# Performance work log

Hardware: AMD Instinct MI355X
Metric: run time of the kernel (lower is better)

The kernel has to match this reference:

```python
import jax, jax.numpy as jnp
import numpy as np

N = 50000      # nodes
E = 800000     # edges (avg degree 16)
D_IN = 128
D_H = 256
NUM_LAYERS = 5


def setup_inputs() -> dict:
    key = jax.random.key(0)
    ks = jax.random.split(key, 12)
    s_in = 1.0 / np.sqrt(D_IN)
    s_h = 1.0 / np.sqrt(D_H)
    x = jax.random.normal(ks[0], (N, D_IN), jnp.float32)
    edge_index = jax.random.randint(ks[1], (2, E), 0, N, jnp.int32)
    eps_all = jnp.zeros((NUM_LAYERS,), jnp.float32)
    # torch Linear layout: weight [out, in], y = x @ W.T + b; scaled for stability
    w0_l0 = jax.random.normal(ks[2], (D_H, D_IN), jnp.float32) * s_in
    b0_l0 = jax.random.normal(ks[3], (D_H,), jnp.float32) * 0.01
    w1_l0 = jax.random.normal(ks[4], (D_H, D_H), jnp.float32) * s_h
    b1_l0 = jax.random.normal(ks[5], (D_H,), jnp.float32) * 0.01
    w0_rest = jax.random.normal(ks[6], (4, D_H, D_H), jnp.float32) * s_h
    b0_rest = jax.random.normal(ks[7], (4, D_H), jnp.float32) * 0.01
    w1_rest = jax.random.normal(ks[8], (4, D_H, D_H), jnp.float32) * s_h
    b1_rest = jax.random.normal(ks[9], (4, D_H), jnp.float32) * 0.01
    return {"x": x, "edge_index": edge_index, "eps_all": eps_all,
            "w0_l0": w0_l0, "b0_l0": b0_l0, "w1_l0": w1_l0, "b1_l0": b1_l0,
            "w0_rest": w0_rest, "b0_rest": b0_rest, "w1_rest": w1_rest, "b1_rest": b1_rest}


def _gin_layer(x, src, dst, eps, w0, b0, w1, b1):
    # gather source-node features along edges, scatter-sum into destination nodes
    aggr = jax.ops.segment_sum(x[src], dst, num_segments=N)  # [N, d]
    h = (1.0 + eps) * x + aggr
    h = jax.nn.relu(h @ w0.T + b0)   # dropout p=0.0 -> identity
    h = h @ w1.T + b1
    return jax.nn.relu(h)            # inter-layer ReLU from the trace


def reference(x, edge_index, eps_all, w0_l0, b0_l0, w1_l0, b1_l0,
              w0_rest, b0_rest, w1_rest, b1_rest):
    src = edge_index[0]  # edge_index_j (messages come from row 0)
    dst = edge_index[1]  # edge_index_i (aggregated at row 1)
    h = _gin_layer(x, src, dst, eps_all[0], w0_l0, b0_l0, w1_l0, b1_l0)
    for i in range(4):  # layers 1..4, identical shapes
        h = _gin_layer(h, src, dst, eps_all[i + 1],
                       w0_rest[i], b0_rest[i], w1_rest[i], b1_rest[i])
    return h  # [N, D_H]
```

## Files before the change

### kernel.cpp

```cpp
#include <hip/hip_runtime.h>
#include <hip/hip_bf16.h>
#include <stdint.h>

#define D_IN 128
#define D_H 256
#define NLAYERS 5

typedef __bf16 bf16x8 __attribute__((ext_vector_type(8)));
typedef float f32x4 __attribute__((ext_vector_type(4)));
typedef unsigned short u16x8 __attribute__((ext_vector_type(8)));

#define MID_STRIDE 260

__device__ inline unsigned short bfbits(float f) {
  __hip_bfloat16 h = __float2bfloat16(f);
  unsigned short s;
  __builtin_memcpy(&s, &h, 2);
  return s;
}

__device__ inline unsigned packbf(float lo, float hi) {
  return (unsigned)bfbits(lo) | ((unsigned)bfbits(hi) << 16);
}

__device__ inline void addbf2(float& a, float& b, unsigned u) {
  a += __uint_as_float(u << 16);
  b += __uint_as_float(u & 0xffff0000u);
}

__device__ inline void addbf2s(float& a, float& b, unsigned u, float s) {
  a += s * __uint_as_float(u << 16);
  b += s * __uint_as_float(u & 0xffff0000u);
}

__global__ void conv_inputs(const float* __restrict__ x, const float* __restrict__ a,
                            const float* __restrict__ b, const float* __restrict__ c,
                            const float* __restrict__ d,
                            __hip_bfloat16* __restrict__ xb,
                            __hip_bfloat16* __restrict__ wb, int nx) {
  int gid = blockIdx.x * blockDim.x + threadIdx.x;
  if (gid < nx) {
    xb[gid] = __float2bfloat16(x[gid]);
    return;
  }
  gid -= nx;
  if (gid >= 622592) return;
  float v;
  if (gid < 32768) v = a[gid];
  else if (gid < 98304) v = b[gid - 32768];
  else if (gid < 360448) v = c[gid - 98304];
  else v = d[gid - 360448];
  wb[gid] = __float2bfloat16(v);
}

__global__ void zero_ints(int* __restrict__ p, int n) {
  int i = blockIdx.x * blockDim.x + threadIdx.x;
  if (i < n) p[i] = 0;
}

__global__ void hist_kernel(const int* __restrict__ ei, int E, int* __restrict__ deg) {
  int e = blockIdx.x * blockDim.x + threadIdx.x;
  if (e < E) atomicAdd(&deg[ei[E + e]], 1);
}

__global__ __launch_bounds__(256) void block_sums(const int* __restrict__ deg,
                                                  int* __restrict__ bsum, int N) {
  int t = threadIdx.x;
  int idx = blockIdx.x * 1024 + t * 4;
  int4 v = {0, 0, 0, 0};
  if (idx + 3 < N) v = *reinterpret_cast<const int4*>(deg + idx);
  else {
    if (idx + 0 < N) v.x = deg[idx + 0];
    if (idx + 1 < N) v.y = deg[idx + 1];
    if (idx + 2 < N) v.z = deg[idx + 2];
    if (idx + 3 < N) v.w = deg[idx + 3];
  }
  int s = v.x + v.y + v.z + v.w;
#pragma unroll
  for (int off = 32; off > 0; off >>= 1) s += __shfl_down(s, off);
  __shared__ int ws[4];
  int lane = t & 63, w = t >> 6;
  if (lane == 0) ws[w] = s;
  __syncthreads();
  if (t == 0) bsum[blockIdx.x] = ws[0] + ws[1] + ws[2] + ws[3];
}

__global__ void scan_bsums(int* __restrict__ bsum, int nb) {
  int t = threadIdx.x;
  int orig = (t < nb) ? bsum[t] : 0;
  int v = orig;
#pragma unroll
  for (int off = 1; off < 64; off <<= 1) {
    int u = __shfl_up(v, off);
    if (t >= off) v += u;
  }
  if (t < nb) bsum[t] = v - orig;
}

__global__ __launch_bounds__(256) void scan_apply(const int* __restrict__ deg,
                                                  const int* __restrict__ bsum_ex,
                                                  int* __restrict__ row_start, int N) {
  int t = threadIdx.x;
  int idx = blockIdx.x * 1024 + t * 4;
  int4 v = {0, 0, 0, 0};
  if (idx + 3 < N) v = *reinterpret_cast<const int4*>(deg + idx);
  else {
    if (idx + 0 < N) v.x = deg[idx + 0];
    if (idx + 1 < N) v.y = deg[idx + 1];
    if (idx + 2 < N) v.z = deg[idx + 2];
    if (idx + 3 < N) v.w = deg[idx + 3];
  }
  int s = v.x + v.y + v.z + v.w;
  int lane = t & 63, w = t >> 6;
  int sc = s;
#pragma unroll
  for (int off = 1; off < 64; off <<= 1) {
    int u = __shfl_up(sc, off);
    if (lane >= off) sc += u;
  }
  __shared__ int woff[4];
  if (lane == 63) woff[w] = sc;
  __syncthreads();
  int boff = bsum_ex[blockIdx.x];
#pragma unroll
  for (int i = 0; i < 4; ++i)
    if (i < w) boff += woff[i];
  int ex = boff + sc - s;
  if (idx + 3 < N) {
    int4 o;
    o.x = ex;
    o.y = ex + v.x;
    o.z = ex + v.x + v.y;
    o.w = ex + v.x + v.y + v.z;
    *reinterpret_cast<int4*>(row_start + idx) = o;
  } else {
    if (idx + 0 < N) row_start[idx + 0] = ex;
    if (idx + 1 < N) row_start[idx + 1] = ex + v.x;
    if (idx + 2 < N) row_start[idx + 2] = ex + v.x + v.y;
    if (idx + 3 < N) row_start[idx + 3] = ex + v.x + v.y + v.z;
  }
}

__global__ void fill_kernel(const int* __restrict__ ei, int E,
                            const int* __restrict__ row_start,
                            int* __restrict__ cursor, int* __restrict__ csr) {
  int e = blockIdx.x * blockDim.x + threadIdx.x;
  if (e >= E) return;
  int d = ei[E + e];
  int p = atomicAdd(&cursor[d], 1);
  csr[row_start[d] + p] = ei[e];
}

template <int D>
__global__ __launch_bounds__(256) void aggregate(const unsigned short* __restrict__ hb,
                                                 const int* __restrict__ csr,
                                                 const int* __restrict__ row_start,
                                                 const int* __restrict__ deg,
                                                 const float* __restrict__ eps_all,
                                                 int layer,
                                                 unsigned short* __restrict__ pre,
                                                 int N) {
  constexpr int PL = D / 32;
  const int half = threadIdx.x >> 5;
  const int lane = threadIdx.x & 31;
  const int node = blockIdx.x * 8 + half;
  if (node >= N) return;

  const int start = row_start[node];
  const int cnt = deg[node];
  const float epsv = 1.0f + eps_all[layer];

  float acc[PL];
#pragma unroll
  for (int j = 0; j < PL; ++j) acc[j] = 0.0f;

  if (D == 256) {
    uint4 su = *reinterpret_cast<const uint4*>(hb + (size_t)node * D + lane * 8);
    for (int base = 0; base < cnt; base += 32) {
      int m = cnt - base;
      if (m > 32) m = 32;
      int idx = (lane < m) ? csr[start + base + lane] : 0;
      int i = 0;
      for (; i + 8 <= m; i += 8) {
        uint4 q[8];
#pragma unroll
        for (int r = 0; r < 8; ++r) {
          int s = __shfl(idx, i + r, 32);
          q[r] = *reinterpret_cast<const uint4*>(hb + (size_t)s * D + lane * 8);
        }
#pragma unroll
        for (int r = 0; r < 8; ++r) {
          addbf2(acc[0], acc[1], q[r].x);
          addbf2(acc[2], acc[3], q[r].y);
          addbf2(acc[4], acc[5], q[r].z);
          addbf2(acc[6], acc[7], q[r].w);
        }
      }
      for (; i + 4 <= m; i += 4) {
        uint4 q[4];
#pragma unroll
        for (int r = 0; r < 4; ++r) {
          int s = __shfl(idx, i + r, 32);
          q[r] = *reinterpret_cast<const uint4*>(hb + (size_t)s * D + lane * 8);
        }
#pragma unroll
        for (int r = 0; r < 4; ++r) {
          addbf2(acc[0], acc[1], q[r].x);
          addbf2(acc[2], acc[3], q[r].y);
          addbf2(acc[4], acc[5], q[r].z);
          addbf2(acc[6], acc[7], q[r].w);
        }
      }
      for (; i < m; ++i) {
        int s = __shfl(idx, i, 32);
        uint4 q = *reinterpret_cast<const uint4*>(hb + (size_t)s * D + lane * 8);
        addbf2(acc[0], acc[1], q.x);
        addbf2(acc[2], acc[3], q.y);
        addbf2(acc[4], acc[5], q.z);
        addbf2(acc[6], acc[7], q.w);
      }
    }
    addbf2s(acc[0], acc[1], su.x, epsv);
    addbf2s(acc[2], acc[3], su.y, epsv);
    addbf2s(acc[4], acc[5], su.z, epsv);
    addbf2s(acc[6], acc[7], su.w, epsv);
    uint4 o;
    o.x = packbf(acc[0], acc[1]);
    o.y = packbf(acc[2], acc[3]);
    o.z = packbf(acc[4], acc[5]);
    o.w = packbf(acc[6], acc[7]);
    *reinterpret_cast<uint4*>(pre + (size_t)node * D + lane * 8) = o;
  } else {
    uint2 su = *reinterpret_cast<const uint2*>(hb + (size_t)node * D + lane * 4);
    for (int base = 0; base < cnt; base += 32) {
      int m = cnt - base;
      if (m > 32) m = 32;
      int idx = (lane < m) ? csr[start + base + lane] : 0;
      int i = 0;
      for (; i + 8 <= m; i += 8) {
        uint2 q[8];
#pragma unroll
        for (int r = 0; r < 8; ++r) {
          int s = __shfl(idx, i + r, 32);
          q[r] = *reinterpret_cast<const uint2*>(hb + (size_t)s * D + lane * 4);
        }
#pragma unroll
        for (int r = 0; r < 8; ++r) {
          addbf2(acc[0], acc[1], q[r].x);
          addbf2(acc[2], acc[3], q[r].y);
        }
      }
      for (; i + 4 <= m; i += 4) {
        uint2 q[4];
#pragma unroll
        for (int r = 0; r < 4; ++r) {
          int s = __shfl(idx, i + r, 32);
          q[r] = *reinterpret_cast<const uint2*>(hb + (size_t)s * D + lane * 4);
        }
#pragma unroll
        for (int r = 0; r < 4; ++r) {
          addbf2(acc[0], acc[1], q[r].x);
          addbf2(acc[2], acc[3], q[r].y);
        }
      }
      for (; i < m; ++i) {
        int s = __shfl(idx, i, 32);
        uint2 q = *reinterpret_cast<const uint2*>(hb + (size_t)s * D + lane * 4);
        addbf2(acc[0], acc[1], q.x);
        addbf2(acc[2], acc[3], q.y);
      }
    }
    addbf2s(acc[0], acc[1], su.x, epsv);
    addbf2s(acc[2], acc[3], su.y, epsv);
    uint2 o;
    o.x = packbf(acc[0], acc[1]);
    o.y = packbf(acc[2], acc[3]);
    *reinterpret_cast<uint2*>(pre + (size_t)node * D + lane * 4) = o;
  }
}

template <int K0, bool OUT_BF16>
__global__ __launch_bounds__(512, 2) void mlp_fused(
    const unsigned short* __restrict__ Ap, const __hip_bfloat16* __restrict__ W0p,
    const float* __restrict__ b0, const __hip_bfloat16* __restrict__ W1p,
    const float* __restrict__ b1, void* __restrict__ Outp, int Nrows) {
  __shared__ unsigned short midb[2][32 * MID_STRIDE];

  constexpr int NK0 = K0 / 32;
  constexpr int NK1 = D_H / 32;
  const int tid = threadIdx.x;
  const int wid = tid >> 6;
  const bool prod = (wid < 4);
  const int cg = wid & 3;
  const int lane = tid & 63;
  const int l15 = lane & 15;
  const int kg = lane >> 4;
  const int col0 = cg * 64;
  const int nch = (Nrows + 31) >> 5;

  bf16x8 wfr[NK1][4];
  float bv[4];
  if (prod) {
    const unsigned short* Ws = (const unsigned short*)W0p;
#pragma unroll
    for (int ct = 0; ct < 4; ++ct) {
      const unsigned short* wrow = Ws + (size_t)(col0 + ct * 16 + l15) * K0 + kg * 8;
#pragma unroll
      for (int kk = 0; kk < NK0; ++kk)
        wfr[kk][ct] = *reinterpret_cast<const bf16x8*>(wrow + kk * 32);
      bv[ct] = b0[col0 + ct * 16 + l15];
    }
  } else {
    const unsigned short* Ws = (const unsigned short*)W1p;
#pragma unroll
    for (int ct = 0; ct < 4; ++ct) {
      const unsigned short* wrow = Ws + (size_t)(col0 + ct * 16 + l15) * D_H + kg * 8;
#pragma unroll
      for (int kk = 0; kk < NK1; ++kk)
        wfr[kk][ct] = *reinterpret_cast<const bf16x8*>(wrow + kk * 32);
      bv[ct] = b1[col0 + ct * 16 + l15];
    }
  }

  auto produce = [&](int c, unsigned short* buf) {
    const int r0 = c << 5;
    bf16x8 afr[NK0][2];
#pragma unroll
    for (int rt = 0; rt < 2; ++rt) {
      int row = r0 + rt * 16 + l15;
      if (row > Nrows - 1) row = Nrows - 1;
      const unsigned short* ar = Ap + (size_t)row * K0 + kg * 8;
#pragma unroll
      for (int kk = 0; kk < NK0; ++kk)
        afr[kk][rt] = *reinterpret_cast<const bf16x8*>(ar + kk * 32);
    }
    f32x4 acc[2][4];
#pragma unroll
    for (int rt = 0; rt < 2; ++rt)
#pragma unroll
      for (int ct = 0; ct < 4; ++ct) acc[rt][ct] = 0.0f;
#pragma unroll
    for (int kk = 0; kk < NK0; ++kk)
#pragma unroll
      for (int rt = 0; rt < 2; ++rt)
#pragma unroll
        for (int ct = 0; ct < 4; ++ct)
          acc[rt][ct] = __builtin_amdgcn_mfma_f32_16x16x32_bf16(
              afr[kk][rt], wfr[kk][ct], acc[rt][ct], 0, 0, 0);
#pragma unroll
    for (int ct = 0; ct < 4; ++ct) {
      int col = col0 + ct * 16 + l15;
#pragma unroll
      for (int rt = 0; rt < 2; ++rt)
#pragma unroll
        for (int i = 0; i < 4; ++i) {
          int row_l = rt * 16 + kg * 4 + i;
          buf[row_l * MID_STRIDE + col] = bfbits(fmaxf(acc[rt][ct][i] + bv[ct], 0.0f));
        }
    }
  };

  auto consume = [&](int c, const unsigned short* buf) {
    const int r0 = c << 5;
    f32x4 acc[2][4];
#pragma unroll
    for (int rt = 0; rt < 2; ++rt)
#pragma unroll
      for (int ct = 0; ct < 4; ++ct) acc[rt][ct] = 0.0f;
#pragma unroll
    for (int kk = 0; kk < NK1; ++kk) {
      bf16x8 mfr[2];
#pragma unroll
      for (int rt = 0; rt < 2; ++rt)
        mfr[rt] = *reinterpret_cast<const bf16x8*>(
            buf + (rt * 16 + l15) * MID_STRIDE + kk * 32 + kg * 8);
#pragma unroll
      for (int rt = 0; rt < 2; ++rt)
#pragma unroll
        for (int ct = 0; ct < 4; ++ct)
          acc[rt][ct] = __builtin_amdgcn_mfma_f32_16x16x32_bf16(
              mfr[rt], wfr[kk][ct], acc[rt][ct], 0, 0, 0);
    }
#pragma unroll
    for (int ct = 0; ct < 4; ++ct) {
      int col = col0 + ct * 16 + l15;
#pragma unroll
      for (int rt = 0; rt < 2; ++rt)
#pragma unroll
        for (int i = 0; i < 4; ++i) {
          int row = r0 + rt * 16 + kg * 4 + i;
          if (row < Nrows) {
            float v = fmaxf(acc[rt][ct][i] + bv[ct], 0.0f);
            if (OUT_BF16)
              ((__hip_bfloat16*)Outp)[(size_t)row * D_H + col] = __float2bfloat16(v);
            else
              ((float*)Outp)[(size_t)row * D_H + col] = v;
          }
        }
    }
  };

  int c_pr = blockIdx.x;
  int c_co = blockIdx.x;
  int pb = 0;
  if (prod && c_pr < nch) produce(c_pr, midb[0]);
  __syncthreads();
  c_pr += gridDim.x;
  while (c_co < nch) {
    if (prod) {
      if (c_pr < nch) produce(c_pr, midb[pb ^ 1]);
    } else {
      consume(c_co, midb[pb]);
    }
    __syncthreads();
    pb ^= 1;
    c_pr += gridDim.x;
    c_co += gridDim.x;
  }
}

extern "C" void kernel_launch(void* const* d_in, const int* in_sizes, int n_in,
                              void* d_out, int out_size, void* d_ws, size_t ws_size,
                              hipStream_t stream) {
  const float* x = (const float*)d_in[0];
  const int* ei = (const int*)d_in[1];
  const float* eps_all = (const float*)d_in[2];
  const float* w0_l0 = (const float*)d_in[3];
  const float* b0_l0 = (const float*)d_in[4];
  const float* w1_l0 = (const float*)d_in[5];
  const float* b1_l0 = (const float*)d_in[6];
  const float* w0_rest = (const float*)d_in[7];
  const float* b0_rest = (const float*)d_in[8];
  const float* w1_rest = (const float*)d_in[9];
  const float* b1_rest = (const float*)d_in[10];

  const int N = in_sizes[0] / D_IN;
  const int E = in_sizes[1] / 2;
  const int NX = N * D_IN;

  char* ws = (char*)d_ws;
  const size_t node_bf = (size_t)N * D_H * sizeof(unsigned short);
  unsigned short* h = (unsigned short*)ws;
  unsigned short* pre = (unsigned short*)(ws + node_bf);
  unsigned short* xb = (unsigned short*)(ws + 2 * node_bf);
  char* p = ws + 2 * node_bf + (size_t)NX * sizeof(unsigned short);
  __hip_bfloat16* wbf = (__hip_bfloat16*)p;
  p += 622592 * sizeof(__hip_bfloat16);
  int* deg = (int*)p;
  int* cursor = deg + N;
  int* row_start = cursor + N;
  int* bsum = row_start + N;
  int* csr = bsum + 64;

  __hip_bfloat16* w0_l0_bf = wbf;
  __hip_bfloat16* w1_l0_bf = wbf + 32768;
  __hip_bfloat16* w0_rest_bf = wbf + 98304;
  __hip_bfloat16* w1_rest_bf = w0_rest_bf + 262144;

  conv_inputs<<<(NX + 622592 + 255) / 256, 256, 0, stream>>>(
      x, w0_l0, w1_l0, w0_rest, w1_rest, (__hip_bfloat16*)xb, wbf, NX);

  const int nb = (N + 1023) / 1024;
  zero_ints<<<(2 * N + 255) / 256, 256, 0, stream>>>(deg, 2 * N);
  hist_kernel<<<(E + 255) / 256, 256, 0, stream>>>(ei, E, deg);
  block_sums<<<nb, 256, 0, stream>>>(deg, bsum, N);
  scan_bsums<<<1, 64, 0, stream>>>(bsum, nb);
  scan_apply<<<nb, 256, 0, stream>>>(deg, bsum, row_start, N);
  fill_kernel<<<(E + 255) / 256, 256, 0, stream>>>(ei, E, row_start, cursor, csr);

  const int mlpGrid = 256;
  const int aggBlocks = (N + 7) / 8;

  for (int layer = 0; layer < NLAYERS; ++layer) {
    const __hip_bfloat16* w0 =
        (layer == 0) ? w0_l0_bf : w0_rest_bf + (size_t)(layer - 1) * 65536;
    const float* b0 = (layer == 0) ? b0_l0 : b0_rest + (size_t)(layer - 1) * 256;
    const __hip_bfloat16* w1 =
        (layer == 0) ? w1_l0_bf : w1_rest_bf + (size_t)(layer - 1) * 65536;
    const float* b1 = (layer == 0) ? b1_l0 : b1_rest + (size_t)(layer - 1) * 256;

    if (layer == 0) {
      aggregate<D_IN><<<aggBlocks, 256, 0, stream>>>(xb, csr, row_start, deg,
                                                     eps_all, layer, pre, N);
      mlp_fused<D_IN, true><<<mlpGrid, 512, 0, stream>>>(pre, w0, b0, w1, b1, h, N);
    } else {
      aggregate<D_H><<<aggBlocks, 256, 0, stream>>>(h, csr, row_start, deg,
                                                    eps_all, layer, pre, N);
      if (layer == NLAYERS - 1)
        mlp_fused<D_H, false><<<mlpGrid, 512, 0, stream>>>(pre, w0, b0, w1, b1,
                                                           d_out, N);
      else
        mlp_fused<D_H, true><<<mlpGrid, 512, 0, stream>>>(pre, w0, b0, w1, b1, h, N);
    }
  }
}
```

Before: 519.7 us.

## Partition CSR histogram and fill by destination range across blocks

The histogram and fill kernels now launch 8 block groups, one per destination-node range. Each group scans all edges with a grid-stride loop and does atomics only for destinations in its own range. The likely aim is to keep each group's atomics and CSR writes within a smaller address window, so they hit cache better, possibly mapping to separate XCDs. In exchange, the edge-destination array is read 8 times and the grid is fixed at 1024 blocks.

```diff
diff --git a/kernel.cpp b/kernel.cpp
--- a/kernel.cpp
+++ b/kernel.cpp
@@ -58,9 +58,39 @@
   if (i < n) p[i] = 0;
 }
 
-__global__ void hist_kernel(const int* __restrict__ ei, int E, int* __restrict__ deg) {
-  int e = blockIdx.x * blockDim.x + threadIdx.x;
-  if (e < E) atomicAdd(&deg[ei[E + e]], 1);
+#define CSR_CHUNKS 128
+
+__global__ __launch_bounds__(256) void hist_kernel(const int* __restrict__ ei, int E,
+                                                   int* __restrict__ deg, int N) {
+  const int r = blockIdx.x & 7;
+  const int chunk = blockIdx.x >> 3;
+  const int rsize = (N + 7) >> 3;
+  const int lo = r * rsize;
+  const int hi = (lo + rsize < N) ? lo + rsize : N;
+  const int stride = CSR_CHUNKS * 256;
+  for (int e = chunk * 256 + threadIdx.x; e < E; e += stride) {
+    int d = ei[E + e];
+    if (d >= lo && d < hi) atomicAdd(&deg[d], 1);
+  }
+}
+
+__global__ __launch_bounds__(256) void fill_kernel(const int* __restrict__ ei, int E,
+                                                   const int* __restrict__ row_start,
+                                                   int* __restrict__ cursor,
+                                                   int* __restrict__ csr, int N) {
+  const int r = blockIdx.x & 7;
+  const int chunk = blockIdx.x >> 3;
+  const int rsize = (N + 7) >> 3;
+  const int lo = r * rsize;
+  const int hi = (lo + rsize < N) ? lo + rsize : N;
+  const int stride = CSR_CHUNKS * 256;
+  for (int e = chunk * 256 + threadIdx.x; e < E; e += stride) {
+    int d = ei[E + e];
+    if (d >= lo && d < hi) {
+      int p = atomicAdd(&cursor[d], 1);
+      csr[row_start[d] + p] = ei[e];
+    }
+  }
 }
 
 __global__ __launch_bounds__(256) void block_sums(const int* __restrict__ deg,
@@ -139,16 +169,6 @@
     if (idx + 2 < N) row_start[idx + 2] = ex + v.x + v.y;
     if (idx + 3 < N) row_start[idx + 3] = ex + v.x + v.y + v.z;
   }
-}
-
-__global__ void fill_kernel(const int* __restrict__ ei, int E,
-                            const int* __restrict__ row_start,
-                            int* __restrict__ cursor, int* __restrict__ csr) {
-  int e = blockIdx.x * blockDim.x + threadIdx.x;
-  if (e >= E) return;
-  int d = ei[E + e];
-  int p = atomicAdd(&cursor[d], 1);
-  csr[row_start[d] + p] = ei[e];
 }
 
 template <int D>
@@ -462,11 +482,11 @@
 
   const int nb = (N + 1023) / 1024;
   zero_ints<<<(2 * N + 255) / 256, 256, 0, stream>>>(deg, 2 * N);
-  hist_kernel<<<(E + 255) / 256, 256, 0, stream>>>(ei, E, deg);
+  hist_kernel<<<8 * CSR_CHUNKS, 256, 0, stream>>>(ei, E, deg, N);
   block_sums<<<nb, 256, 0, stream>>>(deg, bsum, N);
   scan_bsums<<<1, 64, 0, stream>>>(bsum, nb);
   scan_apply<<<nb, 256, 0, stream>>>(deg, bsum, row_start, N);
-  fill_kernel<<<(E + 255) / 256, 256, 0, stream>>>(ei, E, row_start, cursor, csr);
+  fill_kernel<<<8 * CSR_CHUNKS, 256, 0, stream>>>(ei, E, row_start, cursor, csr, N);
 
   const int mlpGrid = 256;
   const int aggBlocks = (N + 7) / 8;
```

After: 509.1 us. -2.0%, faster.
